# Kernel optimization log

Measured on AMD Instinct MI355X. Metric: run time of the kernel, lower is better.

Reference implementation:

```python
import jax, jax.numpy as jnp
import numpy as np

NB, T, N, C = 8, 8, 6890, 128
CLASS_NUM = 7
D_SUM = 512
PCADIM = 64
V = 7702  # garment template vertex count
EPS = 1e-5


def setup_inputs() -> dict:
    key = jax.random.key(0)
    ks = jax.random.split(key, 12)
    f = lambda k, s: jax.random.normal(k, s, dtype=jnp.float32)
    return {
        "x": f(ks[0], (NB, T, N, 3)),
        "sem_logits": f(ks[1], (NB * T, N, CLASS_NUM)),
        "feature": f(ks[2], (NB * T, C, N)),
        "garment_summary": f(ks[3], (NB, T, D_SUM)),
        "W1": f(ks[4], (128, D_SUM)) * 0.02, "b1": jnp.zeros((128,), jnp.float32),
        "g1": jnp.ones((128,), jnp.float32), "be1": jnp.zeros((128,), jnp.float32),
        "rm1": jnp.zeros((128,), jnp.float32), "rv1": jnp.ones((128,), jnp.float32),
        "W2": f(ks[5], (64, 128)) * 0.02, "b2": jnp.zeros((64,), jnp.float32),
        "g2": jnp.ones((64,), jnp.float32), "be2": jnp.zeros((64,), jnp.float32),
        "rm2": jnp.zeros((64,), jnp.float32), "rv2": jnp.ones((64,), jnp.float32),
        "W3": f(ks[6], (PCADIM, 64)) * 0.02, "b3": jnp.zeros((PCADIM,), jnp.float32),
        "pca_comp": f(ks[7], (PCADIM, V * 3)) * 0.02,
        "pca_mean": f(ks[8], (V * 3,)) * 0.02,
        "pca_scale": jnp.abs(f(ks[9], (V * 3,))) + 0.5,
        "garment_label": 1,
        "n": N // 4,
    }


def _segmentation_gather(x, sem_logits, feature, garment_label, n):
    # Vectorized form of the per-sample boolean-mask select / truncate / zero-pad loop.
    # x: [B,N,3]; feature: [B,C,N]; sem_logits: [B,N,K]
    feat = jnp.swapaxes(feature, 1, 2)                     # [B,N,C]
    labels = jnp.argmax(sem_logits, axis=2)                # [B,N] (detached in original)
    mask = labels == garment_label                         # [B,N]
    count = mask.sum(axis=1)                               # [B]
    # stable argsort puts selected (mask=True -> key False=0) indices first, in order
    order = jnp.argsort(jnp.logical_not(mask), axis=1)[:, :n]   # [B,n]
    valid = (jnp.arange(n)[None, :] < count[:, None]).astype(x.dtype)  # [B,n]
    gv = jnp.take_along_axis(x, order[:, :, None], axis=1) * valid[:, :, None]
    gf = jnp.take_along_axis(feat, order[:, :, None], axis=1) * valid[:, :, None]
    return gv, gf


def reference(x, sem_logits, feature, garment_summary, W1, b1, g1, be1, rm1, rv1,
              W2, b2, g2, be2, rm2, rv2, W3, b3, pca_comp, pca_mean, pca_scale,
              garment_label, n):
    nbatch, t = x.shape[0], x.shape[1]
    xf = x.reshape(nbatch * t, -1, 3)
    garment_v, garment_f = _segmentation_gather(xf, sem_logits, feature, garment_label, n)

    # PCAEncoder: 1x1 Conv1d over a length-1 sequence == linear layers; BN in eval mode
    def bn(h, g, be, rm, rv):
        return (h - rm) * jax.lax.rsqrt(rv + EPS) * g + be

    gs = garment_summary.max(axis=1)                       # [nbatch, 512] (max over T)
    h = jax.nn.relu(bn(gs @ W1.T + b1, g1, be1, rm1, rv1))
    h = jax.nn.relu(bn(h @ W2.T + b2, g2, be2, rm2, rv2))
    coeff = h @ W3.T + b3                                  # [nbatch, PCADIM]

    # PCA_inverse_transform
    tpose = ((coeff @ pca_comp) + pca_mean) * pca_scale
    tpose = tpose.reshape(coeff.shape[0], -1, 3)           # [nbatch, V, 3]
    return garment_v, garment_f, coeff, tpose
```

## Files before the change

kernel.cpp:

```cpp
#include <hip/hip_runtime.h>
#include <stdint.h>

#define NBATCH   8
#define TT       8
#define NPTS     6890
#define KCLS     7
#define CCH      128
#define BSAMP    64
#define NOUT     1722
#define DSUM     512
#define PCADIM   64
#define V3       23106
#define EPSBN    1e-5f

#define NW       108
#define PCH      512
#define NCHK     14
#define CHN      32
#define CHB      4
#define LDSR     516
#define CPG      7
#define NGRP     2
#define K4B      91
#define NGATHER  (BSAMP * CHB * NGRP)

#define OFF_GV     0
#define OFF_GF     (BSAMP * NOUT * 3)
#define OFF_COEFF  (OFF_GF + BSAMP * NOUT * CCH)
#define OFF_TPOSE  (OFF_COEFF + NBATCH * PCADIM)

__device__ __forceinline__ void gl_lds16(const float* g, float* l) {
    __builtin_amdgcn_global_load_lds(
        (const __attribute__((address_space(1))) uint32_t*)g,
        (__attribute__((address_space(3))) uint32_t*)l,
        16, 0, 0);
}

__global__ __launch_bounds__(256) void k1_mask_mlp(
    const float* __restrict__ logits,
    const int*   __restrict__ d_label,
    unsigned long long* __restrict__ ws_mask,
    const float* __restrict__ gsum,
    const float* __restrict__ W1, const float* __restrict__ b1,
    const float* __restrict__ g1, const float* __restrict__ be1,
    const float* __restrict__ rm1, const float* __restrict__ rv1,
    const float* __restrict__ W2, const float* __restrict__ b2,
    const float* __restrict__ g2, const float* __restrict__ be2,
    const float* __restrict__ rm2, const float* __restrict__ rv2,
    const float* __restrict__ W3, const float* __restrict__ b3,
    float* __restrict__ coeff_out, float* __restrict__ coeff_ws)
{
    const int tid = threadIdx.x;

    if (blockIdx.x < BSAMP * 27) {
        const int b     = blockIdx.x / 27;
        const int chunk = blockIdx.x % 27;
        const int i     = chunk * 256 + tid;
        const int label = d_label[0];

        bool sel = false;
        if (i < NPTS) {
            const float* p = logits + ((size_t)b * NPTS + i) * KCLS;
            float best = p[0]; int bi = 0;
            #pragma unroll
            for (int k = 1; k < KCLS; ++k) {
                float v = p[k];
                if (v > best) { best = v; bi = k; }
            }
            sel = (bi == label);
        }
        const unsigned long long m = __ballot(sel);
        if ((tid & 63) == 0) {
            const int w = chunk * 4 + (tid >> 6);
            if (w < NW) ws_mask[b * NW + w] = m;
        }
    } else {
        const int s    = blockIdx.x - BSAMP * 27;
        const int lane = tid & 63;
        const int wv   = tid >> 6;

        __shared__ float gs[DSUM];
        __shared__ float h1[128];
        __shared__ float h2[64];

        for (int d = tid; d < DSUM; d += 256) {
            const float* p = gsum + ((size_t)s * TT) * DSUM + d;
            float m = p[0];
            #pragma unroll
            for (int t = 1; t < TT; ++t) m = fmaxf(m, p[(size_t)t * DSUM]);
            gs[d] = m;
        }
        __syncthreads();

        for (int r = 0; r < 32; r += 2) {
            const int j0 = wv * 32 + r, j1 = j0 + 1;
            const float* w0 = W1 + (size_t)j0 * DSUM;
            const float* w1 = W1 + (size_t)j1 * DSUM;
            float pa = 0.f, pb = 0.f;
            #pragma unroll
            for (int d = lane; d < DSUM; d += 64) {
                const float gd = gs[d];
                pa = fmaf(w0[d], gd, pa);
                pb = fmaf(w1[d], gd, pb);
            }
            #pragma unroll
            for (int off = 32; off; off >>= 1) {
                pa += __shfl_xor(pa, off);
                pb += __shfl_xor(pb, off);
            }
            if (lane == 0) {
                pa += b1[j0];
                pa = (pa - rm1[j0]) * rsqrtf(rv1[j0] + EPSBN) * g1[j0] + be1[j0];
                h1[j0] = fmaxf(pa, 0.f);
                pb += b1[j1];
                pb = (pb - rm1[j1]) * rsqrtf(rv1[j1] + EPSBN) * g1[j1] + be1[j1];
                h1[j1] = fmaxf(pb, 0.f);
            }
        }
        __syncthreads();

        for (int r = 0; r < 16; ++r) {
            const int jj = wv * 16 + r;
            const float* w = W2 + (size_t)jj * 128;
            float p = w[lane] * h1[lane] + w[lane + 64] * h1[lane + 64];
            #pragma unroll
            for (int off = 32; off; off >>= 1) p += __shfl_xor(p, off);
            if (lane == 0) {
                p += b2[jj];
                p = (p - rm2[jj]) * rsqrtf(rv2[jj] + EPSBN) * g2[jj] + be2[jj];
                h2[jj] = fmaxf(p, 0.f);
            }
        }
        __syncthreads();

        for (int r = 0; r < 16; ++r) {
            const int jj = wv * 16 + r;
            float p = W3[(size_t)jj * 64 + lane] * h2[lane];
            #pragma unroll
            for (int off = 32; off; off >>= 1) p += __shfl_xor(p, off);
            if (lane == 0) {
                p += b3[jj];
                coeff_out[s * PCADIM + jj] = p;
                coeff_ws[s * PCADIM + jj]  = p;
            }
        }
    }
}

__global__ __launch_bounds__(256, 2) void k2_all(
    const float* __restrict__ feature,
    const unsigned long long* __restrict__ ws_mask,
    const float* __restrict__ x,
    float* __restrict__ gv,
    float* __restrict__ gf,
    const float* __restrict__ coeff_ws,
    const float* __restrict__ comp,
    const float* __restrict__ mean_,
    const float* __restrict__ scale_,
    float* __restrict__ tpose)
{
    __shared__ float lds[CHN * LDSR];
    __shared__ unsigned long long smask[NW];
    __shared__ int  swc[NW];
    __shared__ int  sel_list[8 * 64];
    __shared__ int  s_ns[8];
    __shared__ int  s_cnt;

    const int tid = threadIdx.x;

    if (blockIdx.x < K4B) {
        float* sc = lds;
        for (int o = tid; o < NBATCH * PCADIM; o += 256) sc[o] = coeff_ws[o];
        __syncthreads();

        const int v = blockIdx.x * 256 + tid;
        if (v >= V3) return;

        float acc[NBATCH];
        #pragma unroll
        for (int s = 0; s < NBATCH; ++s) acc[s] = 0.f;
        for (int k = 0; k < PCADIM; ++k) {
            const float pv = comp[(size_t)k * V3 + v];
            #pragma unroll
            for (int s = 0; s < NBATCH; ++s)
                acc[s] = fmaf(sc[s * PCADIM + k], pv, acc[s]);
        }
        const float mn = mean_[v], scl = scale_[v];
        #pragma unroll
        for (int s = 0; s < NBATCH; ++s)
            tpose[(size_t)s * V3 + v] = (acc[s] + mn) * scl;
        return;
    }

    const int gb  = blockIdx.x - K4B;
    const int b   = gb / (CHB * NGRP);
    const int rem = gb % (CHB * NGRP);
    const int cb  = rem / NGRP;
    const int g   = rem % NGRP;
    const int idx = cb * NGRP + g;

    const int lane = tid & 63;
    const int wv   = tid >> 6;
    const float* fbase = feature + ((size_t)b * CCH + cb * CHN) * NPTS;

    if (tid < NW) smask[tid] = ws_mask[b * NW + tid];
    __syncthreads();
    if (tid < NW) swc[tid] = __popcll(smask[tid]);
    __syncthreads();
    if (tid == 0) {
        int run = 0;
        for (int w = 0; w < NW; ++w) { int t = swc[w]; swc[w] = run; run += t; }
        s_cnt = run < NOUT ? run : NOUT;
    }
    __syncthreads();

    {
        const int i0s = idx * 862;
        const int i1s = min(i0s + 862, NPTS);
        const float* xb = x + (size_t)b * NPTS * 3;
        for (int i = i0s + tid; i < i1s; i += 256) {
            const int w = i >> 6, lb6 = i & 63;
            const unsigned long long m = smask[w];
            if ((m >> lb6) & 1ull) {
                const int pos = swc[w] + __popcll(m & ((1ull << lb6) - 1ull));
                if (pos < NOUT) {
                    const size_t go = ((size_t)b * NOUT + pos) * 3;
                    gv[go + 0] = xb[(size_t)i * 3 + 0];
                    gv[go + 1] = xb[(size_t)i * 3 + 1];
                    gv[go + 2] = xb[(size_t)i * 3 + 2];
                }
            }
        }
    }
    {
        const int cnt  = s_cnt;
        const int tail = NOUT - cnt;
        if (tail > 0) {
            const int share = (tail + 7) / 8;
            const int r0    = cnt + idx * share;
            const int r1    = min(r0 + share, NOUT);
            if (r1 > r0) {
                for (int j = r0 + tid; j < r1; j += 256) {
                    float* gp = gv + ((size_t)b * NOUT + j) * 3;
                    gp[0] = 0.f; gp[1] = 0.f; gp[2] = 0.f;
                }
                float4* base4 = (float4*)(gf + ((size_t)b * NOUT + r0) * CCH);
                const int total = (r1 - r0) * 32;
                for (int f = tid; f < total; f += 256)
                    base4[f] = make_float4(0.f, 0.f, 0.f, 0.f);
            }
        }
    }

    #pragma unroll 1
    for (int c = 0; c < CPG; ++c) {
        const int chunk = g * CPG + c;
        const int i0    = chunk * PCH;

        __syncthreads();

        if (chunk != NCHK - 1) {
            #pragma unroll
            for (int it = 0; it < 8; ++it) {
                const int r = wv * 8 + it;
                const float* src = fbase + (size_t)r * NPTS + i0;
                float* dst = &lds[r * LDSR];
                gl_lds16(src + lane * 4,       dst);
                gl_lds16(src + 256 + lane * 4, dst + 256);
            }
        } else {
            const int il = NPTS - i0;
            #pragma unroll
            for (int it = 0; it < 8; ++it) {
                const int r = wv * 8 + it;
                const float* src = fbase + (size_t)r * NPTS + i0;
                for (int off = lane; off < il; off += 64)
                    lds[r * LDSR + off] = src[off];
            }
        }

        #pragma unroll
        for (int j = 0; j < 2; ++j) {
            const int wk   = 2 * wv + j;
            const int word = chunk * 8 + wk;
            unsigned long long m = 0; int base = 0;
            if (word < NW) { m = smask[word]; base = swc[word]; }
            const int sel = (int)((m >> lane) & 1ull);
            const int pos = base + __popcll(m & ((1ull << lane) - 1ull));
            const bool ok = sel && pos < NOUT;
            const unsigned long long mm = __ballot(ok);
            const int before = __popcll(mm & ((1ull << lane) - 1ull));
            if (ok) sel_list[wk * 64 + before] = (wk * 64 + lane) | (pos << 9);
            if (lane == 0) s_ns[wk] = __popcll(mm);
        }

        __syncthreads();

        {
            const int half = lane >> 5;
            const int ch   = lane & 31;
            float* gfb = gf + (size_t)b * NOUT * CCH + cb * CHN + ch;
            #pragma unroll
            for (int j = 0; j < 2; ++j) {
                const int wk = 2 * wv + j;
                const int ns = s_ns[wk];
                int s = half;
                if (s < ns) {
                    int e = sel_list[wk * 64 + s];
                    int p = e & 511, pos = e >> 9;
                    float v = lds[ch * LDSR + p];
                    for (s += 2; s < ns; s += 2) {
                        const int e2 = sel_list[wk * 64 + s];
                        const int p2 = e2 & 511, pos2 = e2 >> 9;
                        const float v2 = lds[ch * LDSR + p2];
                        gfb[(size_t)pos * CCH] = v;
                        v = v2; pos = pos2;
                    }
                    gfb[(size_t)pos * CCH] = v;
                }
            }
        }
    }
}

extern "C" void kernel_launch(void* const* d_in, const int* in_sizes, int n_in,
                              void* d_out, int out_size, void* d_ws, size_t ws_size,
                              hipStream_t stream) {
    const float* x      = (const float*)d_in[0];
    const float* logits = (const float*)d_in[1];
    const float* feat   = (const float*)d_in[2];
    const float* gsum   = (const float*)d_in[3];
    const float* W1  = (const float*)d_in[4];
    const float* b1  = (const float*)d_in[5];
    const float* g1  = (const float*)d_in[6];
    const float* be1 = (const float*)d_in[7];
    const float* rm1 = (const float*)d_in[8];
    const float* rv1 = (const float*)d_in[9];
    const float* W2  = (const float*)d_in[10];
    const float* b2  = (const float*)d_in[11];
    const float* g2  = (const float*)d_in[12];
    const float* be2 = (const float*)d_in[13];
    const float* rm2 = (const float*)d_in[14];
    const float* rv2 = (const float*)d_in[15];
    const float* W3  = (const float*)d_in[16];
    const float* b3  = (const float*)d_in[17];
    const float* comp  = (const float*)d_in[18];
    const float* mean_ = (const float*)d_in[19];
    const float* scale_= (const float*)d_in[20];
    const int* d_label = (const int*)d_in[21];

    float* out   = (float*)d_out;
    float* gv    = out + OFF_GV;
    float* gf    = out + OFF_GF;
    float* coeff = out + OFF_COEFF;
    float* tpose = out + OFF_TPOSE;

    unsigned long long* ws_mask = (unsigned long long*)d_ws;
    float* coeff_ws = (float*)(ws_mask + BSAMP * NW);

    k1_mask_mlp<<<BSAMP * 27 + NBATCH, 256, 0, stream>>>(
        logits, d_label, ws_mask, gsum, W1, b1, g1, be1, rm1, rv1,
        W2, b2, g2, be2, rm2, rv2, W3, b3, coeff, coeff_ws);

    k2_all<<<K4B + NGATHER, 256, 0, stream>>>(
        feat, ws_mask, x, gv, gf, coeff_ws, comp, mean_, scale_, tpose);
}
```

Measured before the change: 101.0 us.

## Move PCA inverse into mask kernel and register-prefetch gather chunks

The PCA inverse transform moves out of the gather kernel into the first kernel. There, 91 extra blocks each recompute the small MLP for all 8 samples redundantly and then produce tpose directly, so the coeff workspace round trip goes away. The gather kernel now uses 16-channel slices with twice as many blocks and higher occupancy (launch bounds 4). It replaces async global_load_lds with float4 register double-buffering that prefetches the next chunk during the current scatter. In exchange, the MLP is computed redundantly 91 times with a serial per-thread dot product, and register pressure rises.

```diff
diff --git a/kernel.cpp b/kernel.cpp
--- a/kernel.cpp
+++ b/kernel.cpp
@@ -16,27 +16,23 @@
 #define NW       108
 #define PCH      512
 #define NCHK     14
-#define CHN      32
-#define CHB      4
+#define CHN      16
+#define CHB      8
+#define NGRP     2
+#define CPG      7
 #define LDSR     516
-#define CPG      7
-#define NGRP     2
-#define K4B      91
 #define NGATHER  (BSAMP * CHB * NGRP)
+
+#define K1MASK   (BSAMP * 27)
+#define K1TP     91
+#define VPB      254
 
 #define OFF_GV     0
 #define OFF_GF     (BSAMP * NOUT * 3)
 #define OFF_COEFF  (OFF_GF + BSAMP * NOUT * CCH)
 #define OFF_TPOSE  (OFF_COEFF + NBATCH * PCADIM)
 
-__device__ __forceinline__ void gl_lds16(const float* g, float* l) {
-    __builtin_amdgcn_global_load_lds(
-        (const __attribute__((address_space(1))) uint32_t*)g,
-        (__attribute__((address_space(3))) uint32_t*)l,
-        16, 0, 0);
-}
-
-__global__ __launch_bounds__(256) void k1_mask_mlp(
+__global__ __launch_bounds__(256) void k1_mask_mlp_tpose(
     const float* __restrict__ logits,
     const int*   __restrict__ d_label,
     unsigned long long* __restrict__ ws_mask,
@@ -48,11 +44,15 @@
     const float* __restrict__ g2, const float* __restrict__ be2,
     const float* __restrict__ rm2, const float* __restrict__ rv2,
     const float* __restrict__ W3, const float* __restrict__ b3,
-    float* __restrict__ coeff_out, float* __restrict__ coeff_ws)
+    const float* __restrict__ comp,
+    const float* __restrict__ mean_,
+    const float* __restrict__ scale_,
+    float* __restrict__ coeff_out,
+    float* __restrict__ tpose)
 {
     const int tid = threadIdx.x;
 
-    if (blockIdx.x < BSAMP * 27) {
+    if (blockIdx.x < K1MASK) {
         const int b     = blockIdx.x / 27;
         const int chunk = blockIdx.x % 27;
         const int i     = chunk * 256 + tid;
@@ -74,90 +74,87 @@
             const int w = chunk * 4 + (tid >> 6);
             if (w < NW) ws_mask[b * NW + w] = m;
         }
-    } else {
-        const int s    = blockIdx.x - BSAMP * 27;
-        const int lane = tid & 63;
-        const int wv   = tid >> 6;
-
-        __shared__ float gs[DSUM];
-        __shared__ float h1[128];
-        __shared__ float h2[64];
-
-        for (int d = tid; d < DSUM; d += 256) {
-            const float* p = gsum + ((size_t)s * TT) * DSUM + d;
-            float m = p[0];
-            #pragma unroll
-            for (int t = 1; t < TT; ++t) m = fmaxf(m, p[(size_t)t * DSUM]);
-            gs[d] = m;
-        }
-        __syncthreads();
-
-        for (int r = 0; r < 32; r += 2) {
-            const int j0 = wv * 32 + r, j1 = j0 + 1;
-            const float* w0 = W1 + (size_t)j0 * DSUM;
-            const float* w1 = W1 + (size_t)j1 * DSUM;
-            float pa = 0.f, pb = 0.f;
-            #pragma unroll
-            for (int d = lane; d < DSUM; d += 64) {
-                const float gd = gs[d];
-                pa = fmaf(w0[d], gd, pa);
-                pb = fmaf(w1[d], gd, pb);
-            }
-            #pragma unroll
-            for (int off = 32; off; off >>= 1) {
-                pa += __shfl_xor(pa, off);
-                pb += __shfl_xor(pb, off);
-            }
-            if (lane == 0) {
-                pa += b1[j0];
-                pa = (pa - rm1[j0]) * rsqrtf(rv1[j0] + EPSBN) * g1[j0] + be1[j0];
-                h1[j0] = fmaxf(pa, 0.f);
-                pb += b1[j1];
-                pb = (pb - rm1[j1]) * rsqrtf(rv1[j1] + EPSBN) * g1[j1] + be1[j1];
-                h1[j1] = fmaxf(pb, 0.f);
-            }
-        }
-        __syncthreads();
-
-        for (int r = 0; r < 16; ++r) {
-            const int jj = wv * 16 + r;
-            const float* w = W2 + (size_t)jj * 128;
-            float p = w[lane] * h1[lane] + w[lane + 64] * h1[lane + 64];
-            #pragma unroll
-            for (int off = 32; off; off >>= 1) p += __shfl_xor(p, off);
-            if (lane == 0) {
-                p += b2[jj];
-                p = (p - rm2[jj]) * rsqrtf(rv2[jj] + EPSBN) * g2[jj] + be2[jj];
-                h2[jj] = fmaxf(p, 0.f);
-            }
-        }
-        __syncthreads();
-
-        for (int r = 0; r < 16; ++r) {
-            const int jj = wv * 16 + r;
-            float p = W3[(size_t)jj * 64 + lane] * h2[lane];
-            #pragma unroll
-            for (int off = 32; off; off >>= 1) p += __shfl_xor(p, off);
-            if (lane == 0) {
-                p += b3[jj];
-                coeff_out[s * PCADIM + jj] = p;
-                coeff_ws[s * PCADIM + jj]  = p;
-            }
-        }
+        return;
+    }
+
+    __shared__ float gs[NBATCH * DSUM];
+    __shared__ float h1[NBATCH * 128];
+    __shared__ float h2[NBATCH * 64];
+    __shared__ float h3[NBATCH * PCADIM];
+
+    for (int o = tid; o < NBATCH * DSUM; o += 256) {
+        const int s = o / DSUM, d = o % DSUM;
+        const float* p = gsum + ((size_t)s * TT) * DSUM + d;
+        float m = p[0];
+        #pragma unroll
+        for (int t = 1; t < TT; ++t) m = fmaxf(m, p[(size_t)t * DSUM]);
+        gs[o] = m;
+    }
+    __syncthreads();
+
+    for (int o = tid; o < NBATCH * 128; o += 256) {
+        const int s = o >> 7, jj = o & 127;
+        const float* w  = W1 + (size_t)jj * DSUM;
+        const float* gp = gs + s * DSUM;
+        float acc = 0.f;
+        for (int d = 0; d < DSUM; ++d) acc = fmaf(w[d], gp[d], acc);
+        acc += b1[jj];
+        acc = (acc - rm1[jj]) * rsqrtf(rv1[jj] + EPSBN) * g1[jj] + be1[jj];
+        h1[o] = fmaxf(acc, 0.f);
+    }
+    __syncthreads();
+
+    for (int o = tid; o < NBATCH * 64; o += 256) {
+        const int s = o >> 6, jj = o & 63;
+        const float* w  = W2 + (size_t)jj * 128;
+        const float* hp = h1 + s * 128;
+        float acc = 0.f;
+        #pragma unroll
+        for (int d = 0; d < 128; ++d) acc = fmaf(w[d], hp[d], acc);
+        acc += b2[jj];
+        acc = (acc - rm2[jj]) * rsqrtf(rv2[jj] + EPSBN) * g2[jj] + be2[jj];
+        h2[o] = fmaxf(acc, 0.f);
+    }
+    __syncthreads();
+
+    for (int o = tid; o < NBATCH * 64; o += 256) {
+        const int s = o >> 6, jj = o & 63;
+        const float* w  = W3 + (size_t)jj * 64;
+        const float* hp = h2 + s * 64;
+        float acc = 0.f;
+        #pragma unroll
+        for (int d = 0; d < 64; ++d) acc = fmaf(w[d], hp[d], acc);
+        acc += b3[jj];
+        h3[o] = acc;
+        if (blockIdx.x == K1MASK) coeff_out[o] = acc;
+    }
+    __syncthreads();
+
+    const int vb = blockIdx.x - K1MASK;
+    #pragma unroll 1
+    for (int v0 = vb * VPB + tid; v0 < min(vb * VPB + VPB, V3); v0 += 256) {
+        float acc[NBATCH];
+        #pragma unroll
+        for (int s = 0; s < NBATCH; ++s) acc[s] = 0.f;
+        for (int k = 0; k < PCADIM; ++k) {
+            const float pv = comp[(size_t)k * V3 + v0];
+            #pragma unroll
+            for (int s = 0; s < NBATCH; ++s)
+                acc[s] = fmaf(h3[s * PCADIM + k], pv, acc[s]);
+        }
+        const float mn = mean_[v0], scl = scale_[v0];
+        #pragma unroll
+        for (int s = 0; s < NBATCH; ++s)
+            tpose[(size_t)s * V3 + v0] = (acc[s] + mn) * scl;
     }
 }
 
-__global__ __launch_bounds__(256, 2) void k2_all(
+__global__ __launch_bounds__(256, 4) void k2_gather(
     const float* __restrict__ feature,
     const unsigned long long* __restrict__ ws_mask,
     const float* __restrict__ x,
     float* __restrict__ gv,
-    float* __restrict__ gf,
-    const float* __restrict__ coeff_ws,
-    const float* __restrict__ comp,
-    const float* __restrict__ mean_,
-    const float* __restrict__ scale_,
-    float* __restrict__ tpose)
+    float* __restrict__ gf)
 {
     __shared__ float lds[CHN * LDSR];
     __shared__ unsigned long long smask[NW];
@@ -166,42 +163,29 @@
     __shared__ int  s_ns[8];
     __shared__ int  s_cnt;
 
-    const int tid = threadIdx.x;
-
-    if (blockIdx.x < K4B) {
-        float* sc = lds;
-        for (int o = tid; o < NBATCH * PCADIM; o += 256) sc[o] = coeff_ws[o];
-        __syncthreads();
-
-        const int v = blockIdx.x * 256 + tid;
-        if (v >= V3) return;
-
-        float acc[NBATCH];
-        #pragma unroll
-        for (int s = 0; s < NBATCH; ++s) acc[s] = 0.f;
-        for (int k = 0; k < PCADIM; ++k) {
-            const float pv = comp[(size_t)k * V3 + v];
-            #pragma unroll
-            for (int s = 0; s < NBATCH; ++s)
-                acc[s] = fmaf(sc[s * PCADIM + k], pv, acc[s]);
-        }
-        const float mn = mean_[v], scl = scale_[v];
-        #pragma unroll
-        for (int s = 0; s < NBATCH; ++s)
-            tpose[(size_t)s * V3 + v] = (acc[s] + mn) * scl;
-        return;
-    }
-
-    const int gb  = blockIdx.x - K4B;
-    const int b   = gb / (CHB * NGRP);
-    const int rem = gb % (CHB * NGRP);
-    const int cb  = rem / NGRP;
-    const int g   = rem % NGRP;
-    const int idx = cb * NGRP + g;
+    const int tid  = threadIdx.x;
+    const int gb   = blockIdx.x;
+    const int b    = gb >> 4;
+    const int idx  = gb & 15;
+    const int cb   = idx >> 1;
+    const int g    = idx & 1;
 
     const int lane = tid & 63;
     const int wv   = tid >> 6;
+    const int p4   = lane * 4;
     const float* fbase = feature + ((size_t)b * CCH + cb * CHN) * NPTS;
+
+    float4 rc[8], rn[8];
+
+    {
+        const int i0 = (g * CPG) * PCH;
+        #pragma unroll
+        for (int it = 0; it < 4; ++it) {
+            const float* src = fbase + (size_t)(wv * 4 + it) * NPTS + i0 + p4;
+            rc[2 * it]     = *(const float4*)(src);
+            rc[2 * it + 1] = *(const float4*)(src + 256);
+        }
+    }
 
     if (tid < NW) smask[tid] = ws_mask[b * NW + tid];
     __syncthreads();
@@ -215,8 +199,8 @@
     __syncthreads();
 
     {
-        const int i0s = idx * 862;
-        const int i1s = min(i0s + 862, NPTS);
+        const int i0s = idx * 431;
+        const int i1s = min(i0s + 431, NPTS);
         const float* xb = x + (size_t)b * NPTS * 3;
         for (int i = i0s + tid; i < i1s; i += 256) {
             const int w = i >> 6, lb6 = i & 63;
@@ -231,12 +215,10 @@
                 }
             }
         }
-    }
-    {
         const int cnt  = s_cnt;
         const int tail = NOUT - cnt;
         if (tail > 0) {
-            const int share = (tail + 7) / 8;
+            const int share = (tail + 15) / 16;
             const int r0    = cnt + idx * share;
             const int r1    = min(r0 + share, NOUT);
             if (r1 > r0) {
@@ -255,27 +237,51 @@
     #pragma unroll 1
     for (int c = 0; c < CPG; ++c) {
         const int chunk = g * CPG + c;
-        const int i0    = chunk * PCH;
+
+        if (c + 1 < CPG) {
+            const int nchunk = chunk + 1;
+            const int i1 = nchunk * PCH;
+            if (nchunk != NCHK - 1) {
+                #pragma unroll
+                for (int it = 0; it < 4; ++it) {
+                    const float* src = fbase + (size_t)(wv * 4 + it) * NPTS + i1 + p4;
+                    rn[2 * it]     = *(const float4*)(src);
+                    rn[2 * it + 1] = *(const float4*)(src + 256);
+                }
+            } else {
+                const int il = NPTS - i1;
+                const int o1 = lane * 2;
+                const int o2 = 128 + lane * 2;
+                #pragma unroll
+                for (int it = 0; it < 4; ++it) {
+                    const float* src = fbase + (size_t)(wv * 4 + it) * NPTS + i1;
+                    float2 a = *(const float2*)(src + o1);
+                    float2 bv = (o2 < il) ? *(const float2*)(src + o2)
+                                          : make_float2(0.f, 0.f);
+                    rn[2 * it] = make_float4(a.x, a.y, bv.x, bv.y);
+                }
+            }
+        }
 
         __syncthreads();
 
         if (chunk != NCHK - 1) {
             #pragma unroll
-            for (int it = 0; it < 8; ++it) {
-                const int r = wv * 8 + it;
-                const float* src = fbase + (size_t)r * NPTS + i0;
-                float* dst = &lds[r * LDSR];
-                gl_lds16(src + lane * 4,       dst);
-                gl_lds16(src + 256 + lane * 4, dst + 256);
+            for (int it = 0; it < 4; ++it) {
+                const int r = wv * 4 + it;
+                *(float4*)(&lds[r * LDSR + p4])       = rc[2 * it];
+                *(float4*)(&lds[r * LDSR + 256 + p4]) = rc[2 * it + 1];
             }
         } else {
-            const int il = NPTS - i0;
-            #pragma unroll
-            for (int it = 0; it < 8; ++it) {
-                const int r = wv * 8 + it;
-                const float* src = fbase + (size_t)r * NPTS + i0;
-                for (int off = lane; off < il; off += 64)
-                    lds[r * LDSR + off] = src[off];
+            const int il = NPTS - chunk * PCH;
+            const int o1 = lane * 2;
+            const int o2 = 128 + lane * 2;
+            #pragma unroll
+            for (int it = 0; it < 4; ++it) {
+                const int r = wv * 4 + it;
+                *(float2*)(&lds[r * LDSR + o1]) = make_float2(rc[2*it].x, rc[2*it].y);
+                if (o2 < il)
+                    *(float2*)(&lds[r * LDSR + o2]) = make_float2(rc[2*it].z, rc[2*it].w);
             }
         }
 
@@ -297,19 +303,19 @@
         __syncthreads();
 
         {
-            const int half = lane >> 5;
-            const int ch   = lane & 31;
+            const int q  = lane >> 4;
+            const int ch = lane & 15;
             float* gfb = gf + (size_t)b * NOUT * CCH + cb * CHN + ch;
             #pragma unroll
             for (int j = 0; j < 2; ++j) {
                 const int wk = 2 * wv + j;
                 const int ns = s_ns[wk];
-                int s = half;
+                int s = q;
                 if (s < ns) {
                     int e = sel_list[wk * 64 + s];
                     int p = e & 511, pos = e >> 9;
                     float v = lds[ch * LDSR + p];
-                    for (s += 2; s < ns; s += 2) {
+                    for (s += 4; s < ns; s += 4) {
                         const int e2 = sel_list[wk * 64 + s];
                         const int p2 = e2 & 511, pos2 = e2 >> 9;
                         const float v2 = lds[ch * LDSR + p2];
@@ -319,6 +325,11 @@
                     gfb[(size_t)pos * CCH] = v;
                 }
             }
+        }
+
+        if (c + 1 < CPG) {
+            #pragma unroll
+            for (int it = 0; it < 8; ++it) rc[it] = rn[it];
         }
     }
 }
@@ -356,12 +367,12 @@
     float* tpose = out + OFF_TPOSE;
 
     unsigned long long* ws_mask = (unsigned long long*)d_ws;
-    float* coeff_ws = (float*)(ws_mask + BSAMP * NW);
-
-    k1_mask_mlp<<<BSAMP * 27 + NBATCH, 256, 0, stream>>>(
+
+    k1_mask_mlp_tpose<<<K1MASK + K1TP, 256, 0, stream>>>(
         logits, d_label, ws_mask, gsum, W1, b1, g1, be1, rm1, rv1,
-        W2, b2, g2, be2, rm2, rv2, W3, b3, coeff, coeff_ws);
-
-    k2_all<<<K4B + NGATHER, 256, 0, stream>>>(
-        feat, ws_mask, x, gv, gf, coeff_ws, comp, mean_, scale_, tpose);
+        W2, b2, g2, be2, rm2, rv2, W3, b3, comp, mean_, scale_,
+        coeff, tpose);
+
+    k2_gather<<<NGATHER, 256, 0, stream>>>(
+        feat, ws_mask, x, gv, gf);
 }
```

After: 198.9 us. +97.0%, slower.

## Register double-buffer feature chunks and halve channel block to double gather blocks

Applied to the files above, without the earlier changes.

Replaces the direct global-to-LDS async loads with register-staged float4 loads that prefetch the next chunk while the current chunk is scattered. It also halves the channels per block (16 instead of 32), doubling the number of gather blocks, and raises the occupancy hint to 4 blocks per CU. Each wavefront now scatters four points in parallel using 16 channel lanes. The intent is to overlap global loads with the scatter and raise parallelism. The cost is more registers for the two buffers and narrower 64-byte gf write segments.

```diff
diff --git a/kernel.cpp b/kernel.cpp
--- a/kernel.cpp
+++ b/kernel.cpp
@@ -16,11 +16,11 @@
 #define NW       108
 #define PCH      512
 #define NCHK     14
-#define CHN      32
-#define CHB      4
+#define CHN      16
+#define CHB      8
+#define NGRP     2
+#define CPG      7
 #define LDSR     516
-#define CPG      7
-#define NGRP     2
 #define K4B      91
 #define NGATHER  (BSAMP * CHB * NGRP)
 
@@ -28,13 +28,6 @@
 #define OFF_GF     (BSAMP * NOUT * 3)
 #define OFF_COEFF  (OFF_GF + BSAMP * NOUT * CCH)
 #define OFF_TPOSE  (OFF_COEFF + NBATCH * PCADIM)
-
-__device__ __forceinline__ void gl_lds16(const float* g, float* l) {
-    __builtin_amdgcn_global_load_lds(
-        (const __attribute__((address_space(1))) uint32_t*)g,
-        (__attribute__((address_space(3))) uint32_t*)l,
-        16, 0, 0);
-}
 
 __global__ __launch_bounds__(256) void k1_mask_mlp(
     const float* __restrict__ logits,
@@ -147,7 +140,7 @@
     }
 }
 
-__global__ __launch_bounds__(256, 2) void k2_all(
+__global__ __launch_bounds__(256, 4) void k2_all(
     const float* __restrict__ feature,
     const unsigned long long* __restrict__ ws_mask,
     const float* __restrict__ x,
@@ -192,16 +185,28 @@
         return;
     }
 
-    const int gb  = blockIdx.x - K4B;
-    const int b   = gb / (CHB * NGRP);
-    const int rem = gb % (CHB * NGRP);
-    const int cb  = rem / NGRP;
-    const int g   = rem % NGRP;
-    const int idx = cb * NGRP + g;
+    const int gb   = blockIdx.x - K4B;
+    const int b    = gb >> 4;
+    const int idx  = gb & 15;
+    const int cb   = idx >> 1;
+    const int g    = idx & 1;
 
     const int lane = tid & 63;
     const int wv   = tid >> 6;
+    const int p4   = lane * 4;
     const float* fbase = feature + ((size_t)b * CCH + cb * CHN) * NPTS;
+
+    float4 rc[8], rn[8];
+
+    {
+        const int i0 = (g * CPG) * PCH;
+        #pragma unroll
+        for (int it = 0; it < 4; ++it) {
+            const float* src = fbase + (size_t)(wv * 4 + it) * NPTS + i0 + p4;
+            rc[2 * it]     = *(const float4*)(src);
+            rc[2 * it + 1] = *(const float4*)(src + 256);
+        }
+    }
 
     if (tid < NW) smask[tid] = ws_mask[b * NW + tid];
     __syncthreads();
@@ -215,8 +220,8 @@
     __syncthreads();
 
     {
-        const int i0s = idx * 862;
-        const int i1s = min(i0s + 862, NPTS);
+        const int i0s = idx * 431;
+        const int i1s = min(i0s + 431, NPTS);
         const float* xb = x + (size_t)b * NPTS * 3;
         for (int i = i0s + tid; i < i1s; i += 256) {
             const int w = i >> 6, lb6 = i & 63;
@@ -231,12 +236,10 @@
                 }
             }
         }
-    }
-    {
         const int cnt  = s_cnt;
         const int tail = NOUT - cnt;
         if (tail > 0) {
-            const int share = (tail + 7) / 8;
+            const int share = (tail + 15) / 16;
             const int r0    = cnt + idx * share;
             const int r1    = min(r0 + share, NOUT);
             if (r1 > r0) {
@@ -255,27 +258,51 @@
     #pragma unroll 1
     for (int c = 0; c < CPG; ++c) {
         const int chunk = g * CPG + c;
-        const int i0    = chunk * PCH;
+
+        if (c + 1 < CPG) {
+            const int nchunk = chunk + 1;
+            const int i1 = nchunk * PCH;
+            if (nchunk != NCHK - 1) {
+                #pragma unroll
+                for (int it = 0; it < 4; ++it) {
+                    const float* src = fbase + (size_t)(wv * 4 + it) * NPTS + i1 + p4;
+                    rn[2 * it]     = *(const float4*)(src);
+                    rn[2 * it + 1] = *(const float4*)(src + 256);
+                }
+            } else {
+                const int il = NPTS - i1;
+                const int o1 = lane * 2;
+                const int o2 = 128 + lane * 2;
+                #pragma unroll
+                for (int it = 0; it < 4; ++it) {
+                    const float* src = fbase + (size_t)(wv * 4 + it) * NPTS + i1;
+                    float2 a = *(const float2*)(src + o1);
+                    float2 bv = (o2 < il) ? *(const float2*)(src + o2)
+                                          : make_float2(0.f, 0.f);
+                    rn[2 * it] = make_float4(a.x, a.y, bv.x, bv.y);
+                }
+            }
+        }
 
         __syncthreads();
 
         if (chunk != NCHK - 1) {
             #pragma unroll
-            for (int it = 0; it < 8; ++it) {
-                const int r = wv * 8 + it;
-                const float* src = fbase + (size_t)r * NPTS + i0;
-                float* dst = &lds[r * LDSR];
-                gl_lds16(src + lane * 4,       dst);
-                gl_lds16(src + 256 + lane * 4, dst + 256);
+            for (int it = 0; it < 4; ++it) {
+                const int r = wv * 4 + it;
+                *(float4*)(&lds[r * LDSR + p4])       = rc[2 * it];
+                *(float4*)(&lds[r * LDSR + 256 + p4]) = rc[2 * it + 1];
             }
         } else {
-            const int il = NPTS - i0;
-            #pragma unroll
-            for (int it = 0; it < 8; ++it) {
-                const int r = wv * 8 + it;
-                const float* src = fbase + (size_t)r * NPTS + i0;
-                for (int off = lane; off < il; off += 64)
-                    lds[r * LDSR + off] = src[off];
+            const int il = NPTS - chunk * PCH;
+            const int o1 = lane * 2;
+            const int o2 = 128 + lane * 2;
+            #pragma unroll
+            for (int it = 0; it < 4; ++it) {
+                const int r = wv * 4 + it;
+                *(float2*)(&lds[r * LDSR + o1]) = make_float2(rc[2*it].x, rc[2*it].y);
+                if (o2 < il)
+                    *(float2*)(&lds[r * LDSR + o2]) = make_float2(rc[2*it].z, rc[2*it].w);
             }
         }
 
@@ -297,19 +324,19 @@
         __syncthreads();
 
         {
-            const int half = lane >> 5;
-            const int ch   = lane & 31;
+            const int q  = lane >> 4;
+            const int ch = lane & 15;
             float* gfb = gf + (size_t)b * NOUT * CCH + cb * CHN + ch;
             #pragma unroll
             for (int j = 0; j < 2; ++j) {
                 const int wk = 2 * wv + j;
                 const int ns = s_ns[wk];
-                int s = half;
+                int s = q;
                 if (s < ns) {
                     int e = sel_list[wk * 64 + s];
                     int p = e & 511, pos = e >> 9;
                     float v = lds[ch * LDSR + p];
-                    for (s += 2; s < ns; s += 2) {
+                    for (s += 4; s < ns; s += 4) {
                         const int e2 = sel_list[wk * 64 + s];
                         const int p2 = e2 & 511, pos2 = e2 >> 9;
                         const float v2 = lds[ch * LDSR + p2];
@@ -319,6 +346,11 @@
                     gfb[(size_t)pos * CCH] = v;
                 }
             }
+        }
+
+        if (c + 1 < CPG) {
+            #pragma unroll
+            for (int it = 0; it < 8; ++it) rc[it] = rn[it];
         }
     }
 }
```

Measured after the change: 97.95 us. 3.0% less time.
